# Optimization experiments

Measured on AMD Instinct MI355X. Metric: run time of the kernel, lower is better.

The kernel has to match this reference:

```python
import jax, jax.numpy as jnp
import numpy as np

N_NODES = 50000
N_EDGES = 800000
D_IN = 128
D_OUT = 128


def setup_inputs() -> dict:
    key = jax.random.key(0)
    k1, k2, k3, k4, k5 = jax.random.split(key, 5)
    # xavier-uniform-like scale for the two linear layers (gain for relu ~ sqrt(2))
    bound = float(np.sqrt(2.0) * np.sqrt(6.0 / (D_IN + D_OUT)))
    return {
        "feat": jax.random.normal(k1, (N_NODES, D_IN), dtype=jnp.float32),
        "w_neigh": jax.random.uniform(k2, (D_OUT, D_IN), minval=-bound, maxval=bound, dtype=jnp.float32),
        "w_self": jax.random.uniform(k3, (D_OUT, D_IN), minval=-bound, maxval=bound, dtype=jnp.float32),
        "b_self": jnp.zeros((D_OUT,), dtype=jnp.float32),
        "rows": jax.random.randint(k4, (N_EDGES,), 0, N_NODES, dtype=jnp.int32),  # src node per edge
        "cols": jax.random.randint(k5, (N_EDGES,), 0, N_NODES, dtype=jnp.int32),  # dst node per edge
    }


def reference(feat, w_neigh, w_self, b_self, rows, cols):
    n = feat.shape[0]
    # srcdata = fc_neigh(feat): [N, D_OUT]
    srcdata = feat @ w_neigh.T
    # deg[j] = A.sum(0)[j] = in-degree of destination j (column sums)
    deg = jax.ops.segment_sum(jnp.ones_like(cols, dtype=feat.dtype), cols, num_segments=n)
    # dstdata = (A @ diag(deg)^-1).T @ srcdata  ==  mean over incoming src neighbors
    agg = jax.ops.segment_sum(srcdata[rows], cols, num_segments=n)  # [N, D_OUT]
    dstdata = agg / jnp.where(deg > 0, deg, 1.0)[:, None]
    # rst = fc_self(h_self) + dstdata
    return feat @ w_self.T + b_self + dstdata
```

## Files before the change

kernel.cpp:

```cpp
#include <hip/hip_runtime.h>

#define D 128
#define CAP 64
#define TILE 16

typedef __attribute__((ext_vector_type(8))) short bf16x8;
typedef __attribute__((ext_vector_type(4))) float floatx4;
typedef __attribute__((ext_vector_type(2))) float floatx2;

__device__ __forceinline__ unsigned short f2bf(float f) {
    unsigned int u = __float_as_uint(f);
    return (unsigned short)((u + 0x7fffu + ((u >> 16) & 1u)) >> 16);
}

__global__ __launch_bounds__(256) void zero_kernel(int* __restrict__ p, int n) {
    int i = blockIdx.x * 256 + threadIdx.x;
    if (i < n) p[i] = 0;
}

__global__ __launch_bounds__(256) void prep_fill_kernel(
    const float* __restrict__ feat,
    const float* __restrict__ w_self,
    const float* __restrict__ w_neigh,
    const int* __restrict__ rows,
    const int* __restrict__ cols,
    unsigned int* __restrict__ feat_q,
    unsigned short* __restrict__ ws_h,
    unsigned short* __restrict__ wn_h,
    int* __restrict__ cursor,
    unsigned short* __restrict__ slots,
    int n_nodes, int n_edges)
{
    const int b = blockIdx.x;
    const int tid = threadIdx.x;
    const int role = b % 3;

    if (role < 2) {
        int pb = (b / 3) * 2 + role;
        int i  = pb * 256 + tid;
        if (i < n_nodes * 32) {
            float4 v = *(const float4*)&feat[(long long)4 * i];
            int q = __builtin_amdgcn_cvt_pk_fp8_f32(v.x, v.y, 0, false);
            q = __builtin_amdgcn_cvt_pk_fp8_f32(v.z, v.w, q, true);
            feat_q[i] = (unsigned int)q;
        }
    } else {
        int fb = b / 3;
        int e  = fb * 256 + tid;
        if (e < n_edges) {
            int c = cols[e];
            int p = atomicAdd(&cursor[c], 1);
            if (p < CAP) slots[c * CAP + p] = (unsigned short)rows[e];
        }
        if (fb < 32) {
            int i = fb * 256 + tid;
            int j = i & 4095;
            const float* src = (i < 4096) ? w_self : w_neigh;
            unsigned short* dst = (i < 4096) ? ws_h : wn_h;
            float4 v = *(const float4*)&src[4 * j];
            ushort4 o;
            o.x = f2bf(v.x); o.y = f2bf(v.y); o.z = f2bf(v.z); o.w = f2bf(v.w);
            *(ushort4*)&dst[4 * j] = o;
        }
    }
}

__global__ __launch_bounds__(256, 6) void agg_gemm_kernel(
    const float* __restrict__ feat,
    const unsigned int* __restrict__ feat_q,
    const int* __restrict__ cursor,
    const unsigned short* __restrict__ slots,
    const unsigned short* __restrict__ ws_h,
    const unsigned short* __restrict__ wn_h,
    const float* __restrict__ b_self,
    float* __restrict__ out,
    int n_nodes)
{
    __shared__ unsigned short s_agg[TILE][136];
    __shared__ int s_deg[TILE];

    const int tid  = threadIdx.x;
    const int row0 = blockIdx.x * TILE;

    if (tid < TILE) {
        int node = row0 + tid;
        int d = 0;
        if (node < n_nodes) {
            d = cursor[node];
            if (d > CAP) d = CAP;
        }
        s_deg[tid] = d;
    }
    __syncthreads();

    {
        const int nl  = tid >> 4;
        const int t16 = tid & 15;
        const int sub = t16 & 1;
        const int ln  = t16 >> 1;
        const int deg = s_deg[nl];
        const int node = row0 + nl;

        float acc[16];
        #pragma unroll
        for (int i = 0; i < 16; ++i) acc[i] = 0.f;

        const unsigned short* slotp = slots + (long long)node * CAP;
        const int sh = sub * 16;

        for (int k0 = 0; k0 < deg; k0 += 16) {
            uint4 s0 = *(const uint4*)(slotp + k0);
            uint4 s1 = *(const uint4*)(slotp + k0 + 8);
            unsigned int sv[8] = {s0.x, s0.y, s0.z, s0.w, s1.x, s1.y, s1.z, s1.w};
            int cnt = deg - k0; if (cnt > 16) cnt = 16;

            uint4 g[8];
            #pragma unroll
            for (int jj = 0; jj < 8; ++jj) {
                int j = jj * 2 + sub;
                int r = (int)((sv[jj] >> sh) & 0xffffu);
                if (j >= cnt) r = node;
                g[jj] = *(const uint4*)(feat_q + (long long)r * 32 + ln * 4);
            }

            #pragma unroll
            for (int jj = 0; jj < 8; ++jj) {
                int j = jj * 2 + sub;
                if (j < cnt) {
                    unsigned int wv[4] = {g[jj].x, g[jj].y, g[jj].z, g[jj].w};
                    #pragma unroll
                    for (int c = 0; c < 4; ++c) {
                        floatx2 lo = __builtin_amdgcn_cvt_pk_f32_fp8((int)wv[c], false);
                        floatx2 hi = __builtin_amdgcn_cvt_pk_f32_fp8((int)wv[c], true);
                        acc[c * 4 + 0] += lo.x;
                        acc[c * 4 + 1] += lo.y;
                        acc[c * 4 + 2] += hi.x;
                        acc[c * 4 + 3] += hi.y;
                    }
                }
            }
        }

        #pragma unroll
        for (int i = 0; i < 16; ++i) acc[i] += __shfl_xor(acc[i], 1);

        if (sub == 0) {
            float inv = (deg > 0) ? 1.0f / (float)deg : 0.0f;
            #pragma unroll
            for (int c = 0; c < 4; ++c) {
                ushort4 o;
                o.x = f2bf(acc[c * 4 + 0] * inv);
                o.y = f2bf(acc[c * 4 + 1] * inv);
                o.z = f2bf(acc[c * 4 + 2] * inv);
                o.w = f2bf(acc[c * 4 + 3] * inv);
                *(ushort4*)&s_agg[nl][ln * 16 + c * 4] = o;
            }
        }
    }

    const int wave  = tid >> 6;
    const int lane  = tid & 63;
    const int m     = lane & 15;
    const int quad  = lane >> 4;
    const int kq    = quad * 8;
    const int cbase = wave * 32;

    floatx4 gacc[2];
    gacc[0] = (floatx4){0.f, 0.f, 0.f, 0.f};
    gacc[1] = (floatx4){0.f, 0.f, 0.f, 0.f};

    int rA = row0 + m;
    if (rA > n_nodes - 1) rA = n_nodes - 1;

    #pragma unroll
    for (int kt = 0; kt < 4; ++kt) {
        const int k = kt * 32 + kq;
        float4 f0 = *(const float4*)&feat[(long long)rA * D + k];
        float4 f1 = *(const float4*)&feat[(long long)rA * D + k + 4];
        bf16x8 a;
        a[0] = (short)f2bf(f0.x); a[1] = (short)f2bf(f0.y);
        a[2] = (short)f2bf(f0.z); a[3] = (short)f2bf(f0.w);
        a[4] = (short)f2bf(f1.x); a[5] = (short)f2bf(f1.y);
        a[6] = (short)f2bf(f1.z); a[7] = (short)f2bf(f1.w);
        #pragma unroll
        for (int nt = 0; nt < 2; ++nt) {
            bf16x8 b = *(const bf16x8*)&ws_h[(cbase + nt * 16 + m) * D + k];
            gacc[nt] = __builtin_amdgcn_mfma_f32_16x16x32_bf16(a, b, gacc[nt], 0, 0, 0);
        }
    }

    __syncthreads();

    #pragma unroll
    for (int kt = 0; kt < 4; ++kt) {
        const int k = kt * 32 + kq;
        bf16x8 a = *(const bf16x8*)&s_agg[m][k];
        #pragma unroll
        for (int nt = 0; nt < 2; ++nt) {
            bf16x8 b = *(const bf16x8*)&wn_h[(cbase + nt * 16 + m) * D + k];
            gacc[nt] = __builtin_amdgcn_mfma_f32_16x16x32_bf16(a, b, gacc[nt], 0, 0, 0);
        }
    }

    #pragma unroll
    for (int nt = 0; nt < 2; ++nt) {
        int col = cbase + nt * 16 + m;
        float bias = b_self[col];
        #pragma unroll
        for (int r = 0; r < 4; ++r) {
            int row = row0 + quad * 4 + r;
            if (row < n_nodes)
                out[(long long)row * D + col] = gacc[nt][r] + bias;
        }
    }
}

extern "C" void kernel_launch(void* const* d_in, const int* in_sizes, int n_in,
                              void* d_out, int out_size, void* d_ws, size_t ws_size,
                              hipStream_t stream) {
    const float* feat    = (const float*)d_in[0];
    const float* w_neigh = (const float*)d_in[1];
    const float* w_self  = (const float*)d_in[2];
    const float* b_self  = (const float*)d_in[3];
    const int*   rows    = (const int*)d_in[4];
    const int*   cols    = (const int*)d_in[5];
    float* out = (float*)d_out;

    const int n_nodes = in_sizes[0] / D;
    const int n_edges = in_sizes[4];

    unsigned int*   feat_q = (unsigned int*)d_ws;
    unsigned short* slots  = (unsigned short*)(feat_q + (size_t)n_nodes * 32);
    int* cursor = (int*)(slots + (size_t)n_nodes * CAP);
    unsigned short* ws_h = (unsigned short*)(cursor + n_nodes);
    unsigned short* wn_h = ws_h + 16384;

    zero_kernel<<<(n_nodes + 255) / 256, 256, 0, stream>>>(cursor, n_nodes);

    int nblocks = (n_nodes * 32 + 255) / 256 + (n_edges + 255) / 256;
    prep_fill_kernel<<<nblocks, 256, 0, stream>>>(
        feat, w_self, w_neigh, rows, cols,
        feat_q, ws_h, wn_h, cursor, slots, n_nodes, n_edges);

    agg_gemm_kernel<<<(n_nodes + TILE - 1) / TILE, 256, 0, stream>>>(
        feat, feat_q, cursor, slots, ws_h, wn_h, b_self, out, n_nodes);
}
```

Measured before the change: 176.0 us.

## Split fused prep kernel into weight-convert, edge-bucketing and feature-quantize kernels

Weight bf16 conversion moves into the cursor-zeroing kernel. The interleaved prep kernel is split into a standalone edge-bucketing kernel, where each thread handles four edges with vectorized int4 loads, and a separate fp8 feature-quantization kernel. This aims to cut per-edge thread overhead and to stop the atomic-heavy bucketing from being mixed with streaming quantization blocks. The cost is one extra kernel launch, and the bucketing and quantization work can no longer overlap within a single grid.

```diff
diff --git a/kernel.cpp b/kernel.cpp
--- a/kernel.cpp
+++ b/kernel.cpp
@@ -13,55 +13,68 @@
     return (unsigned short)((u + 0x7fffu + ((u >> 16) & 1u)) >> 16);
 }
 
-__global__ __launch_bounds__(256) void zero_kernel(int* __restrict__ p, int n) {
-    int i = blockIdx.x * 256 + threadIdx.x;
-    if (i < n) p[i] = 0;
-}
-
-__global__ __launch_bounds__(256) void prep_fill_kernel(
-    const float* __restrict__ feat,
-    const float* __restrict__ w_self,
-    const float* __restrict__ w_neigh,
+__global__ __launch_bounds__(256) void zero_w_kernel(
+    int* __restrict__ cursor, int n_nodes, int nzero,
+    const float* __restrict__ w_self, const float* __restrict__ w_neigh,
+    unsigned short* __restrict__ ws_h, unsigned short* __restrict__ wn_h)
+{
+    const int b = blockIdx.x;
+    const int tid = threadIdx.x;
+    if (b < nzero) {
+        int i = b * 256 + tid;
+        if (i < n_nodes) cursor[i] = 0;
+    } else {
+        int i = (b - nzero) * 256 + tid;
+        int j = i & 4095;
+        const float* src = (i < 4096) ? w_self : w_neigh;
+        unsigned short* dst = (i < 4096) ? ws_h : wn_h;
+        float4 v = *(const float4*)&src[4 * j];
+        ushort4 o;
+        o.x = f2bf(v.x); o.y = f2bf(v.y); o.z = f2bf(v.z); o.w = f2bf(v.w);
+        *(ushort4*)&dst[4 * j] = o;
+    }
+}
+
+__global__ __launch_bounds__(256) void bucket_kernel(
     const int* __restrict__ rows,
     const int* __restrict__ cols,
-    unsigned int* __restrict__ feat_q,
-    unsigned short* __restrict__ ws_h,
-    unsigned short* __restrict__ wn_h,
     int* __restrict__ cursor,
     unsigned short* __restrict__ slots,
-    int n_nodes, int n_edges)
-{
-    const int b = blockIdx.x;
-    const int tid = threadIdx.x;
-    const int role = b % 3;
-
-    if (role < 2) {
-        int pb = (b / 3) * 2 + role;
-        int i  = pb * 256 + tid;
-        if (i < n_nodes * 32) {
-            float4 v = *(const float4*)&feat[(long long)4 * i];
-            int q = __builtin_amdgcn_cvt_pk_fp8_f32(v.x, v.y, 0, false);
-            q = __builtin_amdgcn_cvt_pk_fp8_f32(v.z, v.w, q, true);
-            feat_q[i] = (unsigned int)q;
-        }
-    } else {
-        int fb = b / 3;
-        int e  = fb * 256 + tid;
-        if (e < n_edges) {
+    int n_edges)
+{
+    const int t  = blockIdx.x * 256 + threadIdx.x;
+    const int e0 = t * 4;
+    if (e0 + 3 < n_edges) {
+        int4 c4 = *(const int4*)&cols[e0];
+        int4 r4 = *(const int4*)&rows[e0];
+        int p0 = atomicAdd(&cursor[c4.x], 1);
+        int p1 = atomicAdd(&cursor[c4.y], 1);
+        int p2 = atomicAdd(&cursor[c4.z], 1);
+        int p3 = atomicAdd(&cursor[c4.w], 1);
+        if (p0 < CAP) slots[c4.x * CAP + p0] = (unsigned short)r4.x;
+        if (p1 < CAP) slots[c4.y * CAP + p1] = (unsigned short)r4.y;
+        if (p2 < CAP) slots[c4.z * CAP + p2] = (unsigned short)r4.z;
+        if (p3 < CAP) slots[c4.w * CAP + p3] = (unsigned short)r4.w;
+    } else if (e0 < n_edges) {
+        for (int e = e0; e < n_edges; ++e) {
             int c = cols[e];
             int p = atomicAdd(&cursor[c], 1);
             if (p < CAP) slots[c * CAP + p] = (unsigned short)rows[e];
         }
-        if (fb < 32) {
-            int i = fb * 256 + tid;
-            int j = i & 4095;
-            const float* src = (i < 4096) ? w_self : w_neigh;
-            unsigned short* dst = (i < 4096) ? ws_h : wn_h;
-            float4 v = *(const float4*)&src[4 * j];
-            ushort4 o;
-            o.x = f2bf(v.x); o.y = f2bf(v.y); o.z = f2bf(v.z); o.w = f2bf(v.w);
-            *(ushort4*)&dst[4 * j] = o;
-        }
+    }
+}
+
+__global__ __launch_bounds__(256) void quant_kernel(
+    const float* __restrict__ feat,
+    unsigned int* __restrict__ feat_q,
+    int n_nodes)
+{
+    int i = blockIdx.x * 256 + threadIdx.x;
+    if (i < n_nodes * 32) {
+        float4 v = *(const float4*)&feat[(long long)4 * i];
+        int q = __builtin_amdgcn_cvt_pk_fp8_f32(v.x, v.y, 0, false);
+        q = __builtin_amdgcn_cvt_pk_fp8_f32(v.z, v.w, q, true);
+        feat_q[i] = (unsigned int)q;
     }
 }
 
@@ -235,12 +248,15 @@
     unsigned short* ws_h = (unsigned short*)(cursor + n_nodes);
     unsigned short* wn_h = ws_h + 16384;
 
-    zero_kernel<<<(n_nodes + 255) / 256, 256, 0, stream>>>(cursor, n_nodes);
-
-    int nblocks = (n_nodes * 32 + 255) / 256 + (n_edges + 255) / 256;
-    prep_fill_kernel<<<nblocks, 256, 0, stream>>>(
-        feat, w_self, w_neigh, rows, cols,
-        feat_q, ws_h, wn_h, cursor, slots, n_nodes, n_edges);
+    const int nzero = (n_nodes + 255) / 256;
+    zero_w_kernel<<<nzero + 32, 256, 0, stream>>>(
+        cursor, n_nodes, nzero, w_self, w_neigh, ws_h, wn_h);
+
+    bucket_kernel<<<(n_edges + 1023) / 1024, 256, 0, stream>>>(
+        rows, cols, cursor, slots, n_edges);
+
+    quant_kernel<<<(n_nodes * 32 + 255) / 256, 256, 0, stream>>>(
+        feat, feat_q, n_nodes);
 
     agg_gemm_kernel<<<(n_nodes + TILE - 1) / TILE, 256, 0, stream>>>(
         feat, feat_q, cursor, slots, ws_h, wn_h, b_self, out, n_nodes);
```

After: 179.5 us. No clear change (+2.0%).
